# Optimization experiments

Measured on AMD Instinct MI355X. Metric: run time of the kernel, lower is better.

## Reference

```python
import jax, jax.numpy as jnp
import numpy as np

N_EMBID = 384
N_HEADS = 6
HEAD_SIZE = N_EMBID // N_HEADS
BLOCK_SIZE = 256
EPS = 1e-5


def _layernorm(x, g, b):
    mu = jnp.mean(x, axis=-1, keepdims=True)
    var = jnp.var(x, axis=-1, keepdims=True)
    return (x - mu) * jax.lax.rsqrt(var + EPS) * g + b


def setup_inputs() -> dict:
    key = jax.random.key(0)
    ks = jax.random.split(key, 12)
    B, T, C, H, D = 128, 256, N_EMBID, N_HEADS, HEAD_SIZE
    s_in = 1.0 / np.sqrt(C)
    s_hid = 1.0 / np.sqrt(4 * C)
    return {
        "x": jax.random.normal(ks[0], (B, T, C), dtype=jnp.float32),
        # per-head QKV projections stacked: [H, C, D] (jax convention y = x @ W)
        "wq": jax.random.normal(ks[1], (H, C, D), dtype=jnp.float32) * s_in,
        "wk": jax.random.normal(ks[2], (H, C, D), dtype=jnp.float32) * s_in,
        "wv": jax.random.normal(ks[3], (H, C, D), dtype=jnp.float32) * s_in,
        "w_proj": jax.random.normal(ks[4], (C, C), dtype=jnp.float32) * s_in,
        "b_proj": jnp.zeros((C,), dtype=jnp.float32),
        "w1": jax.random.normal(ks[5], (C, 4 * C), dtype=jnp.float32) * s_in,
        "b1": jnp.zeros((4 * C,), dtype=jnp.float32),
        "w2": jax.random.normal(ks[6], (4 * C, C), dtype=jnp.float32) * s_hid,
        "b2": jnp.zeros((C,), dtype=jnp.float32),
        "ln1_g": jnp.ones((C,), dtype=jnp.float32),
        "ln1_b": jnp.zeros((C,), dtype=jnp.float32),
        "ln2_g": jnp.ones((C,), dtype=jnp.float32),
        "ln2_b": jnp.zeros((C,), dtype=jnp.float32),
    }


def reference(x, wq, wk, wv, w_proj, b_proj, w1, b1, w2, b2,
              ln1_g, ln1_b, ln2_g, ln2_b):
    B, T, C = x.shape
    h = _layernorm(x, ln1_g, ln1_b)
    q = jnp.einsum('btc,hcd->bhtd', h, wq)
    k = jnp.einsum('btc,hcd->bhtd', h, wk)
    v = jnp.einsum('btc,hcd->bhtd', h, wv)
    # NOTE: original scales by C**-0.5 with C = full n_embid, not head_size
    scores = jnp.einsum('bhtd,bhsd->bhts', q, k) * (C ** -0.5)
    causal = jnp.tril(jnp.ones((T, T), dtype=bool))
    scores = jnp.where(causal, scores, -jnp.inf)
    wei = jax.nn.softmax(scores, axis=-1)  # dropout = identity (eval)
    attn = jnp.einsum('bhts,bhsd->bhtd', wei, v)
    attn = attn.transpose(0, 2, 1, 3).reshape(B, T, C)  # concat heads
    x = x + attn @ w_proj + b_proj
    h2 = _layernorm(x, ln2_g, ln2_b)
    mlp = jax.nn.relu(h2 @ w1 + b1) @ w2 + b2
    return x + mlp
```

## Files before the change

### kernel.cpp

```cpp
#include <hip/hip_runtime.h>
#include <stdint.h>

typedef unsigned short u16;
typedef unsigned int u32;
typedef __bf16 bf16x8_t __attribute__((ext_vector_type(8)));
typedef float f32x4_t __attribute__((ext_vector_type(4)));
typedef unsigned int u32x2 __attribute__((ext_vector_type(2)));
typedef unsigned int u32x4 __attribute__((ext_vector_type(4)));

union FragAB { bf16x8_t v; u32x2 q[2]; };
union Frag128 { bf16x8_t v; u32x4 q; };
union Stage16 { u32x4 v; u16 e[8]; };

#define DEVFN static __device__ __forceinline__

DEVFN u16 f2bf(float f) {
    u32 x = __builtin_bit_cast(u32, f);
    return (u16)((x + 0x7fffu + ((x >> 16) & 1u)) >> 16);
}

DEVFN f32x4_t zero4() { f32x4_t z = {0.f, 0.f, 0.f, 0.f}; return z; }

typedef __attribute__((address_space(1))) void as1_void;
typedef __attribute__((address_space(3))) void as3_void;

#define GLOAD_LDS16(src, dst) \
    __builtin_amdgcn_global_load_lds((as1_void*)(void*)(src), (as3_void*)(dst), 16, 0, 0)

#define SCALE_QK 0.051031036307982884f
#define NEG_BIG  -30000.0f

__global__ __launch_bounds__(256) void ln_kernel(
        const float* __restrict__ in, const float* __restrict__ g,
        const float* __restrict__ b, u16* __restrict__ out)
{
    const int lane = threadIdx.x & 63;
    const int w = threadIdx.x >> 6;
    const int row = blockIdx.x * 4 + w;
    const float* rp = in + (size_t)row * 384;
    float v[6];
    float s = 0.f, sq = 0.f;
    #pragma unroll
    for (int j = 0; j < 6; j++) {
        v[j] = rp[lane + j * 64];
        s += v[j];
        sq += v[j] * v[j];
    }
    #pragma unroll
    for (int o = 32; o >= 1; o >>= 1) {
        s  += __shfl_xor(s, o);
        sq += __shfl_xor(sq, o);
    }
    const float mean = s * (1.f / 384.f);
    const float var = sq * (1.f / 384.f) - mean * mean;
    const float rs = rsqrtf(var + 1e-5f);
    u16* op = out + (size_t)row * 384;
    #pragma unroll
    for (int j = 0; j < 6; j++) {
        const int c = lane + j * 64;
        op[c] = f2bf((v[j] - mean) * rs * g[c] + b[c]);
    }
}

__global__ void qkv_w_kernel(const float* __restrict__ wq, const float* __restrict__ wk,
                             const float* __restrict__ wv, u16* __restrict__ bt)
{
    const int idx = blockIdx.x * 256 + threadIdx.x;
    if (idx >= 1152 * 384) return;
    const int j = idx / 384, c = idx % 384;
    const int which = j / 384;
    const int r = j % 384;
    const int h = r / 64, d = r % 64;
    const float* w = (which == 0) ? wq : (which == 1 ? wk : wv);
    bt[idx] = f2bf(w[(h * 384 + c) * 64 + d]);
}

__global__ void transpose_w_kernel(const float* __restrict__ w, u16* __restrict__ bt,
                                   int K, int N)
{
    const int idx = blockIdx.x * 256 + threadIdx.x;
    if (idx >= K * N) return;
    const int n = idx / K, k = idx % K;
    bt[idx] = f2bf(w[(size_t)k * N + n]);
}

template<bool HAS_BIAS, bool HAS_RES, bool RELU, bool OUT_BF16>
__global__ __launch_bounds__(256) void gemm_kernel(
        const u16* __restrict__ A, const u16* __restrict__ Bt,
        const float* __restrict__ bias, const float* __restrict__ res,
        void* __restrict__ Out, int M, int N, int K)
{
    __shared__ u16 As[128 * 64];
    __shared__ u16 Bs[128 * 64];
    const int tid = threadIdx.x;
    const int lane = tid & 63;
    const int w = tid >> 6;
    const int tileN = blockIdx.x * 128;
    const int tileM = blockIdx.y * 128;
    (void)M;

    f32x4_t acc[4][4];
    #pragma unroll
    for (int i = 0; i < 4; i++)
        #pragma unroll
        for (int j = 0; j < 4; j++)
            acc[i][j] = zero4();

    const int m = lane & 15;
    const int g16 = (lane >> 4) * 16;

    for (int k0 = 0; k0 < K; k0 += 64) {
        #pragma unroll
        for (int i = 0; i < 4; i++) {
            const int r = (w * 4 + i) * 8 + (lane >> 3);
            const int sc = (lane & 7) ^ (r & 7);
            GLOAD_LDS16(A + (size_t)(tileM + r) * K + k0 + sc * 8,
                        (char*)As + (w * 4 + i) * 1024);
            GLOAD_LDS16(Bt + (size_t)(tileN + r) * K + k0 + sc * 8,
                        (char*)Bs + (w * 4 + i) * 1024);
        }
        __syncthreads();

        Frag128 af[4][2], bfb[4][2];
        #pragma unroll
        for (int mi = 0; mi < 4; mi++) {
            const int ar = (w >> 1) * 64 + mi * 16 + m;
            const char* rp = (const char*)As + ar * 128;
            const int sw = (ar & 7) << 4;
            #pragma unroll
            for (int ks = 0; ks < 2; ks++)
                af[mi][ks].q = *(const u32x4*)(rp + ((ks * 64 + g16) ^ sw));
        }
        #pragma unroll
        for (int ni = 0; ni < 4; ni++) {
            const int br = (w & 1) * 64 + ni * 16 + m;
            const char* rp = (const char*)Bs + br * 128;
            const int sw = (br & 7) << 4;
            #pragma unroll
            for (int ks = 0; ks < 2; ks++)
                bfb[ni][ks].q = *(const u32x4*)(rp + ((ks * 64 + g16) ^ sw));
        }
        #pragma unroll
        for (int ks = 0; ks < 2; ks++)
            #pragma unroll
            for (int mi = 0; mi < 4; mi++)
                #pragma unroll
                for (int ni = 0; ni < 4; ni++)
                    acc[mi][ni] = __builtin_amdgcn_mfma_f32_16x16x32_bf16(
                        af[mi][ks].v, bfb[ni][ks].v, acc[mi][ni], 0, 0, 0);
        __syncthreads();
    }

    #pragma unroll
    for (int mi = 0; mi < 4; mi++) {
        #pragma unroll
        for (int ni = 0; ni < 4; ni++) {
            #pragma unroll
            for (int r = 0; r < 4; r++) {
                const int grow = tileM + (w >> 1) * 64 + mi * 16 + (lane >> 4) * 4 + r;
                const int gcol = tileN + (w & 1) * 64 + ni * 16 + (lane & 15);
                float v = acc[mi][ni][r];
                if (HAS_BIAS) v += bias[gcol];
                if (HAS_RES) v += res[(size_t)grow * N + gcol];
                if (RELU) v = fmaxf(v, 0.f);
                const size_t o = (size_t)grow * N + gcol;
                if (OUT_BF16) ((u16*)Out)[o] = f2bf(v);
                else ((float*)Out)[o] = v;
            }
        }
    }
}

__global__ __launch_bounds__(256) void attn_kernel(
        const u16* __restrict__ qkv, u16* __restrict__ out, int row0)
{
    __shared__ u16 Kl[256 * 72];
    __shared__ u16 Vt[64 * 264];
    __shared__ u16 Pl[4 * 16 * 264];

    const int bi = blockIdx.x / 6, h = blockIdx.x % 6;
    const int tid = threadIdx.x, lane = tid & 63, w = tid >> 6;
    const u16* base = qkv + (size_t)bi * 256 * 1152 + h * 64;

    #pragma unroll
    for (int pass = 0; pass < 8; pass++) {
        const int s = pass * 32 + (tid >> 3);
        const int d8 = (tid & 7) * 8;
        const u16* krow = base + (size_t)s * 1152;
        *(u32x4*)(&Kl[s * 72 + d8]) = *(const u32x4*)(krow + 384 + d8);
        Stage16 vv;
        vv.v = *(const u32x4*)(krow + 768 + d8);
        #pragma unroll
        for (int j = 0; j < 8; j++) Vt[(d8 + j) * 264 + s] = vv.e[j];
    }
    __syncthreads();

    const int m = lane & 15;
    const int g4 = (lane >> 4) * 4;
    u16* pw = &Pl[w * 16 * 264];

    for (int p = 0; p < 4; p++) {
        const int rt = p * 4 + w;
        const int rp = rt * 16;
        const int nt = rt + 1;

        FragAB qa[2];
        const u16* qrow = base + (size_t)(rp + m) * 1152;
        #pragma unroll
        for (int ks = 0; ks < 2; ks++) {
            qa[ks].q[0] = *(const u32x2*)(qrow + ks * 32 + g4);
            qa[ks].q[1] = *(const u32x2*)(qrow + ks * 32 + 16 + g4);
        }

        f32x4_t sacc[16];
        #pragma unroll
        for (int ct = 0; ct < 16; ct++) {
            if (ct < nt) {
                sacc[ct] = zero4();
                #pragma unroll
                for (int ks = 0; ks < 2; ks++) {
                    FragAB kb;
                    const u16* kr = &Kl[(ct * 16 + m) * 72 + ks * 32 + g4];
                    kb.q[0] = *(const u32x2*)(kr);
                    kb.q[1] = *(const u32x2*)(kr + 16);
                    sacc[ct] = __builtin_amdgcn_mfma_f32_16x16x32_bf16(
                        qa[ks].v, kb.v, sacc[ct], 0, 0, 0);
                }
            }
        }

        const int rbase = rp + (lane >> 4) * 4;
        float mx[4] = {-1e30f, -1e30f, -1e30f, -1e30f};
        #pragma unroll
        for (int ct = 0; ct < 16; ct++) if (ct < nt) {
            #pragma unroll
            for (int r = 0; r < 4; r++) {
                float v = sacc[ct][r] * SCALE_QK;
                if (ct * 16 + m > rbase + r) v = NEG_BIG;
                sacc[ct][r] = v;
                mx[r] = fmaxf(mx[r], v);
            }
        }
        #pragma unroll
        for (int r = 0; r < 4; r++) {
            #pragma unroll
            for (int o = 1; o < 16; o <<= 1) mx[r] = fmaxf(mx[r], __shfl_xor(mx[r], o));
        }
        float sum[4] = {0.f, 0.f, 0.f, 0.f};
        #pragma unroll
        for (int ct = 0; ct < 16; ct++) if (ct < nt) {
            #pragma unroll
            for (int r = 0; r < 4; r++) {
                const float e = __expf(sacc[ct][r] - mx[r]);
                sacc[ct][r] = e;
                sum[r] += e;
            }
        }
        #pragma unroll
        for (int r = 0; r < 4; r++) {
            #pragma unroll
            for (int o = 1; o < 16; o <<= 1) sum[r] += __shfl_xor(sum[r], o);
        }
        float inv[4];
        #pragma unroll
        for (int r = 0; r < 4; r++) inv[r] = 1.f / sum[r];

        #pragma unroll
        for (int ct = 0; ct < 16; ct++) if (ct < nt) {
            #pragma unroll
            for (int r = 0; r < 4; r++)
                pw[((lane >> 4) * 4 + r) * 264 + ct * 16 + m] = f2bf(sacc[ct][r] * inv[r]);
        }
        if (nt & 1) {
            #pragma unroll
            for (int r = 0; r < 4; r++)
                pw[((lane >> 4) * 4 + r) * 264 + nt * 16 + m] = 0;
        }

        const int kpairs = (nt + 1) >> 1;
        f32x4_t oacc[4];
        #pragma unroll
        for (int ni = 0; ni < 4; ni++) oacc[ni] = zero4();
        #pragma unroll
        for (int kk = 0; kk < 8; kk++) if (kk < kpairs) {
            FragAB pa;
            const u16* pr = &pw[m * 264 + kk * 32 + g4];
            pa.q[0] = *(const u32x2*)(pr);
            pa.q[1] = *(const u32x2*)(pr + 16);
            #pragma unroll
            for (int ni = 0; ni < 4; ni++) {
                FragAB vb;
                const u16* vr = &Vt[(ni * 16 + m) * 264 + kk * 32 + g4];
                vb.q[0] = *(const u32x2*)(vr);
                vb.q[1] = *(const u32x2*)(vr + 16);
                oacc[ni] = __builtin_amdgcn_mfma_f32_16x16x32_bf16(
                    pa.v, vb.v, oacc[ni], 0, 0, 0);
            }
        }

        #pragma unroll
        for (int ni = 0; ni < 4; ni++) {
            #pragma unroll
            for (int r = 0; r < 4; r++) {
                const int t = rp + (lane >> 4) * 4 + r;
                out[((size_t)row0 + bi * 256 + t) * 384 + h * 64 + ni * 16 + m] =
                    f2bf(oacc[ni][r]);
            }
        }
    }
}

extern "C" void kernel_launch(void* const* d_in, const int* in_sizes, int n_in,
                              void* d_out, int out_size, void* d_ws, size_t ws_size,
                              hipStream_t stream)
{
    (void)in_sizes; (void)n_in; (void)out_size;
    const float* x     = (const float*)d_in[0];
    const float* wq    = (const float*)d_in[1];
    const float* wk    = (const float*)d_in[2];
    const float* wv    = (const float*)d_in[3];
    const float* wproj = (const float*)d_in[4];
    const float* bproj = (const float*)d_in[5];
    const float* w1    = (const float*)d_in[6];
    const float* b1    = (const float*)d_in[7];
    const float* w2    = (const float*)d_in[8];
    const float* b2    = (const float*)d_in[9];
    const float* ln1g  = (const float*)d_in[10];
    const float* ln1b  = (const float*)d_in[11];
    const float* ln2g  = (const float*)d_in[12];
    const float* ln2b  = (const float*)d_in[13];
    float* out = (float*)d_out;

    char* ws = (char*)d_ws;
    u16* hattn  = (u16*)(ws);
    u16* wqkvT  = (u16*)(ws + 25165824);
    u16* wprojT = (u16*)(ws + 26050560);
    u16* w1T    = (u16*)(ws + 26345472);
    u16* w2T    = (u16*)(ws + 27525120);
    char* dyn   = ws + 28704768;
    const size_t avail = (ws_size > (size_t)28704768) ? ws_size - (size_t)28704768 : (size_t)0;

    int na = 32, nm = 32;
    for (int n = 1; n <= 32; n <<= 1) if ((size_t)75497472  / n <= avail) { na = n; break; }
    for (int n = 1; n <= 32; n <<= 1) if ((size_t)100663296 / n <= avail) { nm = n; break; }

    qkv_w_kernel<<<1728, 256, 0, stream>>>(wq, wk, wv, wqkvT);
    transpose_w_kernel<<<576, 256, 0, stream>>>(wproj, wprojT, 384, 384);
    transpose_w_kernel<<<2304, 256, 0, stream>>>(w1, w1T, 384, 1536);
    transpose_w_kernel<<<2304, 256, 0, stream>>>(w2, w2T, 1536, 384);

    ln_kernel<<<8192, 256, 0, stream>>>(x, ln1g, ln1b, hattn);

    const int rows_a = 32768 / na, bat_a = 128 / na;
    u16* qkvc = (u16*)dyn;
    for (int c = 0; c < na; c++) {
        const int row0 = c * rows_a;
        gemm_kernel<false, false, false, true><<<dim3(9, rows_a / 128), 256, 0, stream>>>(
            hattn + (size_t)row0 * 384, wqkvT, nullptr, nullptr, qkvc, rows_a, 1152, 384);
        attn_kernel<<<bat_a * 6, 256, 0, stream>>>(qkvc, hattn, row0);
    }

    gemm_kernel<true, true, false, false><<<dim3(3, 256), 256, 0, stream>>>(
        hattn, wprojT, bproj, x, out, 32768, 384, 384);

    ln_kernel<<<8192, 256, 0, stream>>>(out, ln2g, ln2b, hattn);

    const int rows_m = 32768 / nm;
    u16* mlp1c = (u16*)dyn;
    for (int c = 0; c < nm; c++) {
        const int row0 = c * rows_m;
        gemm_kernel<true, false, true, true><<<dim3(12, rows_m / 128), 256, 0, stream>>>(
            hattn + (size_t)row0 * 384, w1T, b1, nullptr, mlp1c, rows_m, 1536, 384);
        gemm_kernel<true, true, false, false><<<dim3(3, rows_m / 128), 256, 0, stream>>>(
            mlp1c, w2T, b2, out + (size_t)row0 * 384, out + (size_t)row0 * 384,
            rows_m, 384, 1536);
    }
}
```

Measured before the change: 453.1 us.

## Keep softmax probabilities in registers by computing transposed S = K·Q^T

Swaps the MFMA operands so each lane holds a query row's scores across key positions. Softmax max and sum then reduce with two cross-lane shuffles instead of four per row, and the normalized probabilities are packed into bf16 A-fragments directly from registers. This removes the per-wave LDS P buffer along with its stores and reloads, and loads Q and K fragments as single 128-bit reads. In exchange it relies on the K-dimension fragment layout of the 16x16x32 MFMA matching the packed register order, and correctness depends on that mapping being consistent for the P·V multiply.

```diff
diff --git a/kernel.cpp b/kernel.cpp
--- a/kernel.cpp
+++ b/kernel.cpp
@@ -17,6 +17,10 @@
 DEVFN u16 f2bf(float f) {
     u32 x = __builtin_bit_cast(u32, f);
     return (u16)((x + 0x7fffu + ((x >> 16) & 1u)) >> 16);
+}
+
+DEVFN u32 pack2bf(float a, float b) {
+    return (u32)f2bf(a) | ((u32)f2bf(b) << 16);
 }
 
 DEVFN f32x4_t zero4() { f32x4_t z = {0.f, 0.f, 0.f, 0.f}; return z; }
@@ -176,7 +180,6 @@
 {
     __shared__ u16 Kl[256 * 72];
     __shared__ u16 Vt[64 * 264];
-    __shared__ u16 Pl[4 * 16 * 264];
 
     const int bi = blockIdx.x / 6, h = blockIdx.x % 6;
     const int tid = threadIdx.x, lane = tid & 63, w = tid >> 6;
@@ -197,20 +200,19 @@
 
     const int m = lane & 15;
     const int g4 = (lane >> 4) * 4;
-    u16* pw = &Pl[w * 16 * 264];
+    const int g8e = (lane >> 4) * 8;
 
     for (int p = 0; p < 4; p++) {
         const int rt = p * 4 + w;
         const int rp = rt * 16;
         const int nt = rt + 1;
-
-        FragAB qa[2];
-        const u16* qrow = base + (size_t)(rp + m) * 1152;
-        #pragma unroll
-        for (int ks = 0; ks < 2; ks++) {
-            qa[ks].q[0] = *(const u32x2*)(qrow + ks * 32 + g4);
-            qa[ks].q[1] = *(const u32x2*)(qrow + ks * 32 + 16 + g4);
-        }
+        const int qg = rp + m;
+
+        Frag128 qb[2];
+        const u16* qrow = base + (size_t)qg * 1152;
+        #pragma unroll
+        for (int ks = 0; ks < 2; ks++)
+            qb[ks].q = *(const u32x4*)(qrow + ks * 32 + g8e);
 
         f32x4_t sacc[16];
         #pragma unroll
@@ -219,63 +221,41 @@
                 sacc[ct] = zero4();
                 #pragma unroll
                 for (int ks = 0; ks < 2; ks++) {
-                    FragAB kb;
-                    const u16* kr = &Kl[(ct * 16 + m) * 72 + ks * 32 + g4];
-                    kb.q[0] = *(const u32x2*)(kr);
-                    kb.q[1] = *(const u32x2*)(kr + 16);
+                    Frag128 kb;
+                    kb.q = *(const u32x4*)(&Kl[(ct * 16 + m) * 72 + ks * 32 + g8e]);
                     sacc[ct] = __builtin_amdgcn_mfma_f32_16x16x32_bf16(
-                        qa[ks].v, kb.v, sacc[ct], 0, 0, 0);
+                        kb.v, qb[ks].v, sacc[ct], 0, 0, 0);
                 }
             }
         }
 
-        const int rbase = rp + (lane >> 4) * 4;
-        float mx[4] = {-1e30f, -1e30f, -1e30f, -1e30f};
+        float mx = -1e30f;
         #pragma unroll
         for (int ct = 0; ct < 16; ct++) if (ct < nt) {
             #pragma unroll
             for (int r = 0; r < 4; r++) {
                 float v = sacc[ct][r] * SCALE_QK;
-                if (ct * 16 + m > rbase + r) v = NEG_BIG;
+                if (ct * 16 + g4 + r > qg) v = NEG_BIG;
                 sacc[ct][r] = v;
-                mx[r] = fmaxf(mx[r], v);
-            }
-        }
-        #pragma unroll
-        for (int r = 0; r < 4; r++) {
-            #pragma unroll
-            for (int o = 1; o < 16; o <<= 1) mx[r] = fmaxf(mx[r], __shfl_xor(mx[r], o));
-        }
-        float sum[4] = {0.f, 0.f, 0.f, 0.f};
+                mx = fmaxf(mx, v);
+            }
+        }
+        mx = fmaxf(mx, __shfl_xor(mx, 16));
+        mx = fmaxf(mx, __shfl_xor(mx, 32));
+
+        float sum = 0.f;
         #pragma unroll
         for (int ct = 0; ct < 16; ct++) if (ct < nt) {
             #pragma unroll
             for (int r = 0; r < 4; r++) {
-                const float e = __expf(sacc[ct][r] - mx[r]);
+                const float e = __expf(sacc[ct][r] - mx);
                 sacc[ct][r] = e;
-                sum[r] += e;
-            }
-        }
-        #pragma unroll
-        for (int r = 0; r < 4; r++) {
-            #pragma unroll
-            for (int o = 1; o < 16; o <<= 1) sum[r] += __shfl_xor(sum[r], o);
-        }
-        float inv[4];
-        #pragma unroll
-        for (int r = 0; r < 4; r++) inv[r] = 1.f / sum[r];
-
-        #pragma unroll
-        for (int ct = 0; ct < 16; ct++) if (ct < nt) {
-            #pragma unroll
-            for (int r = 0; r < 4; r++)
-                pw[((lane >> 4) * 4 + r) * 264 + ct * 16 + m] = f2bf(sacc[ct][r] * inv[r]);
-        }
-        if (nt & 1) {
-            #pragma unroll
-            for (int r = 0; r < 4; r++)
-                pw[((lane >> 4) * 4 + r) * 264 + nt * 16 + m] = 0;
-        }
+                sum += e;
+            }
+        }
+        sum += __shfl_xor(sum, 16);
+        sum += __shfl_xor(sum, 32);
+        const float inv = 1.f / sum;
 
         const int kpairs = (nt + 1) >> 1;
         f32x4_t oacc[4];
@@ -284,9 +264,19 @@
         #pragma unroll
         for (int kk = 0; kk < 8; kk++) if (kk < kpairs) {
             FragAB pa;
-            const u16* pr = &pw[m * 264 + kk * 32 + g4];
-            pa.q[0] = *(const u32x2*)(pr);
-            pa.q[1] = *(const u32x2*)(pr + 16);
+            {
+                const f32x4_t p0 = sacc[2 * kk];
+                pa.q[0][0] = pack2bf(p0[0] * inv, p0[1] * inv);
+                pa.q[0][1] = pack2bf(p0[2] * inv, p0[3] * inv);
+            }
+            if (2 * kk + 1 < nt) {
+                const f32x4_t p1 = sacc[2 * kk + 1];
+                pa.q[1][0] = pack2bf(p1[0] * inv, p1[1] * inv);
+                pa.q[1][1] = pack2bf(p1[2] * inv, p1[3] * inv);
+            } else {
+                pa.q[1][0] = 0u;
+                pa.q[1][1] = 0u;
+            }
             #pragma unroll
             for (int ni = 0; ni < 4; ni++) {
                 FragAB vb;
```

New measurement: 445.7 us. Within noise of the previous version (-1.6%).
